# Kernel optimization log

Measured on AMD Instinct MI355X. Metric: run time of the kernel, lower is better.

The kernel has to match this reference:

```python
import jax, jax.numpy as jnp
import numpy as np

B, C, H, W = 256, 512, 14, 14  # C = rnn_size
S = 7                          # spp_size

def setup_inputs() -> dict:
    key = jax.random.key(0)
    ks = jax.random.split(key, 8)
    sd = 1.0 / np.sqrt(C)
    return {
        "att_v": jax.random.normal(ks[0], (B, C, H, W), dtype=jnp.float32),
        "h": jax.random.normal(ks[1], (B, C), dtype=jnp.float32),
        # a2a: Linear(rnn_size, rnn_size)
        "Wa": jax.random.uniform(ks[2], (C, C), jnp.float32, -sd, sd),
        "ba": jax.random.uniform(ks[3], (C,), jnp.float32, -sd, sd),
        # h2a: Linear(rnn_size, rnn_size)
        "Wh": jax.random.uniform(ks[4], (C, C), jnp.float32, -sd, sd),
        "bh": jax.random.uniform(ks[5], (C,), jnp.float32, -sd, sd),
        # d2d: Linear(rnn_size, 1)
        "Wd": jax.random.uniform(ks[6], (C,), jnp.float32, -sd, sd),
        "bd": jax.random.uniform(ks[7], (1,), jnp.float32, -sd, sd),
    }

def reference(att_v, h, Wa, ba, Wh, bh, Wd, bd):
    b, c, hh, ww = att_v.shape
    # AdaptiveAvgPool2d(S) with H,W divisible by S -> block mean
    pooled = att_v.reshape(b, c, S, hh // S, S, ww // S).mean(axis=(3, 5))  # [B,C,S,S]
    a = pooled.reshape(b, c, S * S).transpose(0, 2, 1)  # [B, N=49, C]
    av = jnp.einsum('bnc,dc->bnd', a, Wa) + ba          # a2a, torch Linear: x @ W.T + b
    ah = h @ Wh.T + bh                                  # h2a, [B,C]
    dot = jnp.tanh(av + ah[:, None, :])                 # broadcast add + tanh
    scores = jnp.einsum('bnd,d->bn', dot, Wd) + bd[0]   # d2d -> [B, N]
    weight = jax.nn.softmax(scores, axis=-1)            # over attention positions
    att_res = jnp.einsum('bnc,bn->bc', a, weight)       # bmm(att^T, weight)
    return att_res
```

## Files before the change

kernel.cpp:

```cpp
#include <hip/hip_runtime.h>
#include <hip/hip_bf16.h>

#define BATCH 256
#define CDIM  512
#define NPOS  49
#define MROWS 12544
#define ASTRIDE 520

typedef __attribute__((ext_vector_type(8))) short bf16x8_t;
typedef __attribute__((ext_vector_type(4))) float f32x4_t;

#define WS_NEED 14730240u

__device__ __forceinline__ void load_lds16(const void* g, void* l) {
    __builtin_amdgcn_global_load_lds(
        (const __attribute__((address_space(1))) void*)g,
        (__attribute__((address_space(3))) void*)l, 16, 0, 0);
}

__global__ __launch_bounds__(256) void prep(
    const float* __restrict__ Wa, const float* __restrict__ Wh,
    const float* __restrict__ h,
    __hip_bfloat16* __restrict__ Wab, __hip_bfloat16* __restrict__ Whb,
    __hip_bfloat16* __restrict__ hb, float* __restrict__ scores) {
    int gid = blockIdx.x * 256 + threadIdx.x;
    if (gid >= 166976) return;
    if (gid < 163840) {
        const float* src; __hip_bfloat16* dst; int idx;
        if (gid < 65536)       { src = Wa; dst = Wab; idx = gid; }
        else if (gid < 131072) { src = Wh; dst = Whb; idx = gid - 65536; }
        else                   { src = h;  dst = hb;  idx = gid - 131072; }
        float4 v = ((const float4*)src)[idx];
        dst[idx * 4 + 0] = __float2bfloat16(v.x);
        dst[idx * 4 + 1] = __float2bfloat16(v.y);
        dst[idx * 4 + 2] = __float2bfloat16(v.z);
        dst[idx * 4 + 3] = __float2bfloat16(v.w);
    } else {
        int idx = gid - 163840;
        ((float4*)scores)[idx] = (float4){0.f, 0.f, 0.f, 0.f};
    }
}

__global__ __launch_bounds__(256, 6) void pool_kernel(
    const float* __restrict__ att_v, __hip_bfloat16* __restrict__ pooled) {
    __shared__ float4 lds[32 * 49];
    const int b  = blockIdx.x >> 4;
    const int cg = blockIdx.x & 15;
    const int t  = threadIdx.x;

    const float4* src = (const float4*)(att_v + ((size_t)b * CDIM + cg * 32) * 196);
    #pragma unroll
    for (int k = 0; k < 7; ++k) {
        int idx = t + k * 256;
        if (idx < 1568) lds[idx] = src[idx];
    }
    __syncthreads();

    const int i = t >> 5;
    const int c = t & 31;
    if (i < 7) {
        const float4* fp = &lds[c * 49 + 7 * i];
        float4 f0 = fp[0], f1 = fp[1], f2 = fp[2], f3 = fp[3];
        float4 f4 = fp[4], f5 = fp[5], f6 = fp[6];
        float p[7];
        p[0] = f0.x + f0.y + f3.z + f3.w;
        p[1] = f0.z + f0.w + f4.x + f4.y;
        p[2] = f1.x + f1.y + f4.z + f4.w;
        p[3] = f1.z + f1.w + f5.x + f5.y;
        p[4] = f2.x + f2.y + f5.z + f5.w;
        p[5] = f2.z + f2.w + f6.x + f6.y;
        p[6] = f3.x + f3.y + f6.z + f6.w;
        __hip_bfloat16* outp = pooled + ((size_t)b * NPOS + i * 7) * CDIM + cg * 32 + c;
        #pragma unroll
        for (int j = 0; j < 7; ++j)
            outp[(size_t)j * CDIM] = __float2bfloat16(p[j] * 0.25f);
    }
}

__global__ __launch_bounds__(256, 2) void ah_gemm(
    const __hip_bfloat16* __restrict__ A,
    const __hip_bfloat16* __restrict__ Bw,
    const float* __restrict__ ba, const float* __restrict__ bh,
    float* __restrict__ ahb) {
    __shared__ __hip_bfloat16 aT[128 * 32];
    __shared__ __hip_bfloat16 bT[128 * 32];
    const int mt = blockIdx.x & 1;
    const int nt = blockIdx.x >> 1;
    const int t = threadIdx.x;
    const int wave = t >> 6, lane = t & 63;
    const int wm = wave & 1, wn = wave >> 1;
    const int q = lane >> 4, r = lane & 15;
    const int m0 = mt * 128, n0 = nt * 128;

    const __hip_bfloat16* Ag = A + (size_t)(m0 + wave * 16 + (lane >> 2)) * CDIM + (lane & 3) * 8;
    const __hip_bfloat16* Bg = Bw + (size_t)(n0 + wave * 16 + (lane >> 2)) * CDIM + (lane & 3) * 8;
    char* aD = (char*)aT + wave * 1024 + lane * 16;
    char* bD = (char*)bT + wave * 1024 + lane * 16;

    f32x4_t acc[4][4];
    #pragma unroll
    for (int rt = 0; rt < 4; ++rt)
        #pragma unroll
        for (int ct = 0; ct < 4; ++ct) acc[rt][ct] = (f32x4_t){0.f, 0.f, 0.f, 0.f};

    for (int ks = 0; ks < 16; ++ks) {
        const __hip_bfloat16* ag = Ag + ks * 32;
        const __hip_bfloat16* bg = Bg + ks * 32;
        load_lds16(ag, aD);
        load_lds16(ag + 64 * CDIM, aD + 4096);
        load_lds16(bg, bD);
        load_lds16(bg + 64 * CDIM, bD + 4096);
        __syncthreads();
        bf16x8_t af[4], bf[4];
        #pragma unroll
        for (int rt = 0; rt < 4; ++rt)
            af[rt] = *(const bf16x8_t*)&aT[(wm * 64 + rt * 16 + r) * 32 + q * 8];
        #pragma unroll
        for (int ct = 0; ct < 4; ++ct)
            bf[ct] = *(const bf16x8_t*)&bT[(wn * 64 + ct * 16 + r) * 32 + q * 8];
        #pragma unroll
        for (int rt = 0; rt < 4; ++rt)
            #pragma unroll
            for (int ct = 0; ct < 4; ++ct)
                acc[rt][ct] = __builtin_amdgcn_mfma_f32_16x16x32_bf16(
                    af[rt], bf[ct], acc[rt][ct], 0, 0, 0);
        __syncthreads();
    }
    #pragma unroll
    for (int ct = 0; ct < 4; ++ct) {
        const int col = n0 + wn * 64 + ct * 16 + r;
        const float bias = ba[col] + bh[col];
        #pragma unroll
        for (int rt = 0; rt < 4; ++rt)
            #pragma unroll
            for (int rg = 0; rg < 4; ++rg) {
                const int row = m0 + wm * 64 + rt * 16 + q * 4 + rg;
                ahb[(size_t)row * CDIM + col] = acc[rt][ct][rg] + bias;
            }
    }
}

__global__ __launch_bounds__(256, 2) void gemm_score2(
    const __hip_bfloat16* __restrict__ A,
    const __hip_bfloat16* __restrict__ Bw,
    const float* __restrict__ ahb,
    const float* __restrict__ Wd,
    float* __restrict__ scores) {
    __shared__ __hip_bfloat16 aT[128 * 32];
    __shared__ __hip_bfloat16 bT[128 * 32];
    const int mt = blockIdx.x % 98;
    const int nt = blockIdx.x / 98;
    const int t = threadIdx.x;
    const int wave = t >> 6, lane = t & 63;
    const int wm = wave & 1, wn = wave >> 1;
    const int q = lane >> 4, r = lane & 15;
    const int m0 = mt * 128, n0 = nt * 128;

    const __hip_bfloat16* Ag = A + (size_t)(m0 + wave * 16 + (lane >> 2)) * CDIM + (lane & 3) * 8;
    const __hip_bfloat16* Bg = Bw + (size_t)(n0 + wave * 16 + (lane >> 2)) * CDIM + (lane & 3) * 8;
    char* aD = (char*)aT + wave * 1024 + lane * 16;
    char* bD = (char*)bT + wave * 1024 + lane * 16;

    f32x4_t acc[4][4];
    #pragma unroll
    for (int rt = 0; rt < 4; ++rt)
        #pragma unroll
        for (int ct = 0; ct < 4; ++ct) acc[rt][ct] = (f32x4_t){0.f, 0.f, 0.f, 0.f};

    for (int ks = 0; ks < 16; ++ks) {
        const __hip_bfloat16* ag = Ag + ks * 32;
        const __hip_bfloat16* bg = Bg + ks * 32;
        load_lds16(ag, aD);
        load_lds16(ag + 64 * CDIM, aD + 4096);
        load_lds16(bg, bD);
        load_lds16(bg + 64 * CDIM, bD + 4096);
        __syncthreads();
        bf16x8_t af[4], bf[4];
        #pragma unroll
        for (int rt = 0; rt < 4; ++rt)
            af[rt] = *(const bf16x8_t*)&aT[(wm * 64 + rt * 16 + r) * 32 + q * 8];
        #pragma unroll
        for (int ct = 0; ct < 4; ++ct)
            bf[ct] = *(const bf16x8_t*)&bT[(wn * 64 + ct * 16 + r) * 32 + q * 8];
        #pragma unroll
        for (int rt = 0; rt < 4; ++rt)
            #pragma unroll
            for (int ct = 0; ct < 4; ++ct)
                acc[rt][ct] = __builtin_amdgcn_mfma_f32_16x16x32_bf16(
                    af[rt], bf[ct], acc[rt][ct], 0, 0, 0);
        __syncthreads();
    }

    int bb[16];
    #pragma unroll
    for (int rt = 0; rt < 4; ++rt)
        #pragma unroll
        for (int rg = 0; rg < 4; ++rg)
            bb[rt * 4 + rg] = (m0 + wm * 64 + rt * 16 + q * 4 + rg) / NPOS;

    float rsum[16];
    #pragma unroll
    for (int i = 0; i < 16; ++i) rsum[i] = 0.f;

    #pragma unroll
    for (int ct = 0; ct < 4; ++ct) {
        const int col = n0 + wn * 64 + ct * 16 + r;
        const float wd = Wd[col];
        #pragma unroll
        for (int rt = 0; rt < 4; ++rt)
            #pragma unroll
            for (int rg = 0; rg < 4; ++rg) {
                float x = acc[rt][ct][rg] + ahb[(size_t)bb[rt * 4 + rg] * CDIM + col];
                float e = __expf(2.f * x);
                rsum[rt * 4 + rg] += (1.f - 2.f / (e + 1.f)) * wd;
            }
    }
    #pragma unroll
    for (int m = 1; m < 16; m <<= 1)
        #pragma unroll
        for (int i = 0; i < 16; ++i)
            rsum[i] += __shfl_xor(rsum[i], m, 64);
    if (r == 0) {
        #pragma unroll
        for (int rt = 0; rt < 4; ++rt)
            #pragma unroll
            for (int rg = 0; rg < 4; ++rg)
                atomicAdd(&scores[m0 + wm * 64 + rt * 16 + q * 4 + rg],
                          rsum[rt * 4 + rg]);
    }
}

__global__ __launch_bounds__(256) void softmax_wsum(
    const float* __restrict__ scores, const __hip_bfloat16* __restrict__ pooled,
    float* __restrict__ out) {
    const int b  = blockIdx.x >> 1;
    const int ch = (blockIdx.x & 1) * 256 + threadIdx.x;
    const float* sp = scores + b * NPOS;
    float vmax = -3.0e38f;
    #pragma unroll
    for (int n = 0; n < NPOS; ++n) vmax = fmaxf(vmax, sp[n]);
    const __hip_bfloat16* Ap = pooled + (size_t)b * NPOS * CDIM + ch;
    float sum = 0.f, accv = 0.f;
    #pragma unroll
    for (int n = 0; n < NPOS; ++n) {
        float e = __expf(sp[n] - vmax);
        sum += e;
        accv += e * __bfloat162float(Ap[(size_t)n * CDIM]);
    }
    out[b * CDIM + ch] = accv / sum;
}

__global__ void prep_convert(const float* __restrict__ Wa,
                             const float* __restrict__ Wh,
                             __hip_bfloat16* __restrict__ Wab,
                             __hip_bfloat16* __restrict__ Whb) {
    int gid = blockIdx.x * blockDim.x + threadIdx.x;
    const int quarter = (CDIM * CDIM) / 4;
    const float4* src; __hip_bfloat16* dst; int idx;
    if (gid < quarter) { src = (const float4*)Wa; dst = Wab; idx = gid; }
    else               { src = (const float4*)Wh; dst = Whb; idx = gid - quarter; }
    float4 v = src[idx];
    dst[idx * 4 + 0] = __float2bfloat16(v.x);
    dst[idx * 4 + 1] = __float2bfloat16(v.y);
    dst[idx * 4 + 2] = __float2bfloat16(v.z);
    dst[idx * 4 + 3] = __float2bfloat16(v.w);
}

__global__ __launch_bounds__(512, 2) void att_spp_main(
    const float* __restrict__ att_v, const float* __restrict__ h,
    const float* __restrict__ ba, const float* __restrict__ bh,
    const float* __restrict__ Wd,
    const __hip_bfloat16* __restrict__ Wab, const __hip_bfloat16* __restrict__ Whb,
    float* __restrict__ out) {
    __shared__ __hip_bfloat16 a_lds[64 * ASTRIDE];
    __shared__ __hip_bfloat16 h_lds[CDIM];
    __shared__ float babh_lds[CDIM];
    __shared__ float wd_lds[CDIM];
    __shared__ float scores_lds[64];
    __shared__ float weights_lds[NPOS];
    const int b = blockIdx.x, t = threadIdx.x;
    h_lds[t]    = __float2bfloat16(h[b * CDIM + t]);
    babh_lds[t] = ba[t] + bh[t];
    wd_lds[t]   = Wd[t];
    if (t < 64) scores_lds[t] = 0.f;
    for (int idx = t; idx < (64 - NPOS) * ASTRIDE; idx += 512)
        a_lds[NPOS * ASTRIDE + idx] = __float2bfloat16(0.f);
    {
        const int jj = t & 7, g = t >> 3;
        const float2* att2 = (const float2*)(att_v + (size_t)b * CDIM * 196);
        if (jj < 7) {
            for (int ci = 0; ci < 8; ++ci) {
                const int c = g + (ci << 6), cbase = c * 98;
                #pragma unroll
                for (int i = 0; i < 7; ++i) {
                    float2 v0 = att2[cbase + i * 14 + jj];
                    float2 v1 = att2[cbase + i * 14 + 7 + jj];
                    a_lds[(i * 7 + jj) * ASTRIDE + c] =
                        __float2bfloat16((v0.x + v0.y + v1.x + v1.y) * 0.25f);
                }
            }
        }
    }
    __syncthreads();
    const int wave = t >> 6, lane = t & 63, q = lane >> 4, r = lane & 15;
    f32x4_t acc[4][4];
    #pragma unroll
    for (int rt = 0; rt < 4; ++rt)
        #pragma unroll
        for (int ct = 0; ct < 4; ++ct) acc[rt][ct] = (f32x4_t){0.f,0.f,0.f,0.f};
    const int dBase = wave * 64 + r;
    for (int ks = 0; ks < 16; ++ks) {
        const int k0 = ks * 32 + q * 8;
        bf16x8_t af[4], bf[4];
        #pragma unroll
        for (int rt = 0; rt < 4; ++rt)
            af[rt] = *(const bf16x8_t*)&a_lds[(rt * 16 + r) * ASTRIDE + k0];
        #pragma unroll
        for (int ct = 0; ct < 4; ++ct)
            bf[ct] = *(const bf16x8_t*)&Wab[(size_t)(dBase + ct * 16) * CDIM + k0];
        #pragma unroll
        for (int rt = 0; rt < 4; ++rt)
            #pragma unroll
            for (int ct = 0; ct < 4; ++ct)
                acc[rt][ct] = __builtin_amdgcn_mfma_f32_16x16x32_bf16(
                    af[rt], bf[ct], acc[rt][ct], 0, 0, 0);
    }
    for (int ks = 0; ks < 16; ++ks) {
        const int k0 = ks * 32 + q * 8;
        bf16x8_t af = *(const bf16x8_t*)&h_lds[k0];
        bf16x8_t bf[4];
        #pragma unroll
        for (int ct = 0; ct < 4; ++ct)
            bf[ct] = *(const bf16x8_t*)&Whb[(size_t)(dBase + ct * 16) * CDIM + k0];
        #pragma unroll
        for (int rt = 0; rt < 4; ++rt)
            #pragma unroll
            for (int ct = 0; ct < 4; ++ct)
                acc[rt][ct] = __builtin_amdgcn_mfma_f32_16x16x32_bf16(
                    af, bf[ct], acc[rt][ct], 0, 0, 0);
    }
    float part[4][4];
    #pragma unroll
    for (int rt = 0; rt < 4; ++rt)
        #pragma unroll
        for (int rg = 0; rg < 4; ++rg) part[rt][rg] = 0.f;
    #pragma unroll
    for (int ct = 0; ct < 4; ++ct) {
        const int d = dBase + ct * 16;
        const float bias = babh_lds[d], wd = wd_lds[d];
        #pragma unroll
        for (int rt = 0; rt < 4; ++rt)
            #pragma unroll
            for (int rg = 0; rg < 4; ++rg) {
                float x = acc[rt][ct][rg] + bias;
                float e = __expf(2.f * x);
                part[rt][rg] += (1.f - 2.f / (e + 1.f)) * wd;
            }
    }
    #pragma unroll
    for (int m = 1; m < 16; m <<= 1)
        #pragma unroll
        for (int rt = 0; rt < 4; ++rt)
            #pragma unroll
            for (int rg = 0; rg < 4; ++rg)
                part[rt][rg] += __shfl_xor(part[rt][rg], m, 64);
    if (r == 0) {
        #pragma unroll
        for (int rt = 0; rt < 4; ++rt)
            #pragma unroll
            for (int rg = 0; rg < 4; ++rg)
                atomicAdd(&scores_lds[rt * 16 + q * 4 + rg], part[rt][rg]);
    }
    __syncthreads();
    if (wave == 0) {
        float v = (lane < NPOS) ? scores_lds[lane] : -3.0e38f;
        float vmax = v;
        #pragma unroll
        for (int m = 1; m < 64; m <<= 1) vmax = fmaxf(vmax, __shfl_xor(vmax, m, 64));
        float e = (lane < NPOS) ? __expf(v - vmax) : 0.f;
        float s = e;
        #pragma unroll
        for (int m = 1; m < 64; m <<= 1) s += __shfl_xor(s, m, 64);
        if (lane < NPOS) weights_lds[lane] = e / s;
    }
    __syncthreads();
    float sum = 0.f;
    #pragma unroll
    for (int n = 0; n < NPOS; ++n)
        sum += __bfloat162float(a_lds[n * ASTRIDE + t]) * weights_lds[n];
    out[b * CDIM + t] = sum;
}

extern "C" void kernel_launch(void* const* d_in, const int* in_sizes, int n_in,
                              void* d_out, int out_size, void* d_ws, size_t ws_size,
                              hipStream_t stream) {
    const float* att_v = (const float*)d_in[0];
    const float* h     = (const float*)d_in[1];
    const float* Wa    = (const float*)d_in[2];
    const float* ba    = (const float*)d_in[3];
    const float* Wh    = (const float*)d_in[4];
    const float* bh    = (const float*)d_in[5];
    const float* Wd    = (const float*)d_in[6];

    if (ws_size >= WS_NEED) {
        char* ws = (char*)d_ws;
        __hip_bfloat16* Wab    = (__hip_bfloat16*)(ws);
        __hip_bfloat16* Whb    = (__hip_bfloat16*)(ws + 524288);
        __hip_bfloat16* hb     = (__hip_bfloat16*)(ws + 1048576);
        __hip_bfloat16* pooled = (__hip_bfloat16*)(ws + 1310720);
        float*          ahb    = (float*)(ws + 14155776);
        float*          scores = (float*)(ws + 14680064);

        prep<<<653, 256, 0, stream>>>(Wa, Wh, h, Wab, Whb, hb, scores);
        pool_kernel<<<4096, 256, 0, stream>>>(att_v, pooled);
        ah_gemm<<<8, 256, 0, stream>>>(hb, Whb, ba, bh, ahb);
        gemm_score2<<<392, 256, 0, stream>>>(pooled, Wab, ahb, Wd, scores);
        softmax_wsum<<<512, 256, 0, stream>>>(scores, pooled, (float*)d_out);
    } else {
        __hip_bfloat16* Wab = (__hip_bfloat16*)d_ws;
        __hip_bfloat16* Whb = Wab + (size_t)CDIM * CDIM;
        prep_convert<<<512, 256, 0, stream>>>(Wa, Wh, Wab, Whb);
        att_spp_main<<<BATCH, 512, 0, stream>>>(att_v, h, ba, bh, Wd, Wab, Whb,
                                                (float*)d_out);
    }
}
```

Baseline: 200.6 us.

## Tile score GEMM per batch and replace atomics with partial-score buffers

The score GEMM now uses one 64-row tile per batch (49 valid rows) across 4 N-tiles, so each block reads a single ah row instead of gathering per-row batch indices. Atomics into a zeroed scores array are replaced by 8 per-wave-column partial segments that the softmax kernel sums into LDS, which removes the zeroing pass from prep. The ah GEMM switches to 64x64 tiles so it runs on 32 blocks instead of 8. The cost is padding 49 rows up to 64, about 23% wasted MFMA and load work, plus a larger workspace.

```diff
diff --git a/kernel.cpp b/kernel.cpp
--- a/kernel.cpp
+++ b/kernel.cpp
@@ -10,7 +10,7 @@
 typedef __attribute__((ext_vector_type(8))) short bf16x8_t;
 typedef __attribute__((ext_vector_type(4))) float f32x4_t;
 
-#define WS_NEED 14730240u
+#define WS_NEED 15081472u
 
 __device__ __forceinline__ void load_lds16(const void* g, void* l) {
     __builtin_amdgcn_global_load_lds(
@@ -22,23 +22,17 @@
     const float* __restrict__ Wa, const float* __restrict__ Wh,
     const float* __restrict__ h,
     __hip_bfloat16* __restrict__ Wab, __hip_bfloat16* __restrict__ Whb,
-    __hip_bfloat16* __restrict__ hb, float* __restrict__ scores) {
+    __hip_bfloat16* __restrict__ hb) {
     int gid = blockIdx.x * 256 + threadIdx.x;
-    if (gid >= 166976) return;
-    if (gid < 163840) {
-        const float* src; __hip_bfloat16* dst; int idx;
-        if (gid < 65536)       { src = Wa; dst = Wab; idx = gid; }
-        else if (gid < 131072) { src = Wh; dst = Whb; idx = gid - 65536; }
-        else                   { src = h;  dst = hb;  idx = gid - 131072; }
-        float4 v = ((const float4*)src)[idx];
-        dst[idx * 4 + 0] = __float2bfloat16(v.x);
-        dst[idx * 4 + 1] = __float2bfloat16(v.y);
-        dst[idx * 4 + 2] = __float2bfloat16(v.z);
-        dst[idx * 4 + 3] = __float2bfloat16(v.w);
-    } else {
-        int idx = gid - 163840;
-        ((float4*)scores)[idx] = (float4){0.f, 0.f, 0.f, 0.f};
-    }
+    const float* src; __hip_bfloat16* dst; int idx;
+    if (gid < 65536)       { src = Wa; dst = Wab; idx = gid; }
+    else if (gid < 131072) { src = Wh; dst = Whb; idx = gid - 65536; }
+    else                   { src = h;  dst = hb;  idx = gid - 131072; }
+    float4 v = ((const float4*)src)[idx];
+    dst[idx * 4 + 0] = __float2bfloat16(v.x);
+    dst[idx * 4 + 1] = __float2bfloat16(v.y);
+    dst[idx * 4 + 2] = __float2bfloat16(v.z);
+    dst[idx * 4 + 3] = __float2bfloat16(v.w);
 }
 
 __global__ __launch_bounds__(256, 6) void pool_kernel(
@@ -77,173 +71,176 @@
     }
 }
 
-__global__ __launch_bounds__(256, 2) void ah_gemm(
+__global__ __launch_bounds__(256, 4) void ah_gemm(
     const __hip_bfloat16* __restrict__ A,
     const __hip_bfloat16* __restrict__ Bw,
     const float* __restrict__ ba, const float* __restrict__ bh,
     float* __restrict__ ahb) {
-    __shared__ __hip_bfloat16 aT[128 * 32];
-    __shared__ __hip_bfloat16 bT[128 * 32];
-    const int mt = blockIdx.x & 1;
-    const int nt = blockIdx.x >> 1;
+    __shared__ __hip_bfloat16 aT[64 * 32];
+    __shared__ __hip_bfloat16 bT[64 * 32];
+    const int mt = blockIdx.x & 3;
+    const int nt = blockIdx.x >> 2;
     const int t = threadIdx.x;
     const int wave = t >> 6, lane = t & 63;
     const int wm = wave & 1, wn = wave >> 1;
     const int q = lane >> 4, r = lane & 15;
-    const int m0 = mt * 128, n0 = nt * 128;
-
-    const __hip_bfloat16* Ag = A + (size_t)(m0 + wave * 16 + (lane >> 2)) * CDIM + (lane & 3) * 8;
-    const __hip_bfloat16* Bg = Bw + (size_t)(n0 + wave * 16 + (lane >> 2)) * CDIM + (lane & 3) * 8;
-    char* aD = (char*)aT + wave * 1024 + lane * 16;
-    char* bD = (char*)bT + wave * 1024 + lane * 16;
-
-    f32x4_t acc[4][4];
-    #pragma unroll
-    for (int rt = 0; rt < 4; ++rt)
+    const int m0 = mt * 64, n0 = nt * 64;
+
+    const __hip_bfloat16* Ag = A + (size_t)(m0 + (t >> 2)) * CDIM + (t & 3) * 8;
+    const __hip_bfloat16* Bg = Bw + (size_t)(n0 + (t >> 2)) * CDIM + (t & 3) * 8;
+    char* aD = (char*)aT + t * 16;
+    char* bD = (char*)bT + t * 16;
+
+    f32x4_t acc[2][2];
+    #pragma unroll
+    for (int rt = 0; rt < 2; ++rt)
+        #pragma unroll
+        for (int ct = 0; ct < 2; ++ct) acc[rt][ct] = (f32x4_t){0.f, 0.f, 0.f, 0.f};
+
+    for (int ks = 0; ks < 16; ++ks) {
+        load_lds16(Ag + ks * 32, aD);
+        load_lds16(Bg + ks * 32, bD);
+        __syncthreads();
+        bf16x8_t af[2], bf[2];
+        #pragma unroll
+        for (int rt = 0; rt < 2; ++rt)
+            af[rt] = *(const bf16x8_t*)&aT[(wm * 32 + rt * 16 + r) * 32 + q * 8];
+        #pragma unroll
+        for (int ct = 0; ct < 2; ++ct)
+            bf[ct] = *(const bf16x8_t*)&bT[(wn * 32 + ct * 16 + r) * 32 + q * 8];
+        #pragma unroll
+        for (int rt = 0; rt < 2; ++rt)
+            #pragma unroll
+            for (int ct = 0; ct < 2; ++ct)
+                acc[rt][ct] = __builtin_amdgcn_mfma_f32_16x16x32_bf16(
+                    af[rt], bf[ct], acc[rt][ct], 0, 0, 0);
+        __syncthreads();
+    }
+    #pragma unroll
+    for (int ct = 0; ct < 2; ++ct) {
+        const int col = n0 + wn * 32 + ct * 16 + r;
+        const float bias = ba[col] + bh[col];
+        #pragma unroll
+        for (int rt = 0; rt < 2; ++rt)
+            #pragma unroll
+            for (int rg = 0; rg < 4; ++rg) {
+                const int row = m0 + wm * 32 + rt * 16 + q * 4 + rg;
+                ahb[(size_t)row * CDIM + col] = acc[rt][ct][rg] + bias;
+            }
+    }
+}
+
+__global__ __launch_bounds__(256, 4) void gemm_score3(
+    const __hip_bfloat16* __restrict__ A,
+    const __hip_bfloat16* __restrict__ Bw,
+    const float* __restrict__ ahb,
+    const float* __restrict__ Wd,
+    float* __restrict__ scores8) {
+    __shared__ __hip_bfloat16 aT[64 * 32];
+    __shared__ __hip_bfloat16 bT[128 * 32];
+    const int b  = blockIdx.x >> 2;
+    const int nt = blockIdx.x & 3;
+    const int t = threadIdx.x;
+    const int wave = t >> 6, lane = t & 63;
+    const int wm = wave & 1, wn = wave >> 1;
+    const int q = lane >> 4, r = lane & 15;
+    const int m0 = b * NPOS;
+    const int n0 = nt * 128;
+
+    const __hip_bfloat16* Ag = A + (size_t)(m0 + (t >> 2)) * CDIM + (t & 3) * 8;
+    const __hip_bfloat16* Bg = Bw + (size_t)(n0 + (t >> 2)) * CDIM + (t & 3) * 8;
+    char* aD = (char*)aT + t * 16;
+    char* bD = (char*)bT + t * 16;
+
+    f32x4_t acc[2][4];
+    #pragma unroll
+    for (int rt = 0; rt < 2; ++rt)
         #pragma unroll
         for (int ct = 0; ct < 4; ++ct) acc[rt][ct] = (f32x4_t){0.f, 0.f, 0.f, 0.f};
 
     for (int ks = 0; ks < 16; ++ks) {
-        const __hip_bfloat16* ag = Ag + ks * 32;
-        const __hip_bfloat16* bg = Bg + ks * 32;
-        load_lds16(ag, aD);
-        load_lds16(ag + 64 * CDIM, aD + 4096);
-        load_lds16(bg, bD);
-        load_lds16(bg + 64 * CDIM, bD + 4096);
+        load_lds16(Ag + ks * 32, aD);
+        load_lds16(Bg + ks * 32, bD);
+        load_lds16(Bg + (size_t)64 * CDIM + ks * 32, bD + 4096);
         __syncthreads();
-        bf16x8_t af[4], bf[4];
-        #pragma unroll
-        for (int rt = 0; rt < 4; ++rt)
-            af[rt] = *(const bf16x8_t*)&aT[(wm * 64 + rt * 16 + r) * 32 + q * 8];
+        bf16x8_t af[2], bf[4];
+        #pragma unroll
+        for (int rt = 0; rt < 2; ++rt)
+            af[rt] = *(const bf16x8_t*)&aT[(wm * 32 + rt * 16 + r) * 32 + q * 8];
         #pragma unroll
         for (int ct = 0; ct < 4; ++ct)
             bf[ct] = *(const bf16x8_t*)&bT[(wn * 64 + ct * 16 + r) * 32 + q * 8];
         #pragma unroll
-        for (int rt = 0; rt < 4; ++rt)
+        for (int rt = 0; rt < 2; ++rt)
             #pragma unroll
             for (int ct = 0; ct < 4; ++ct)
                 acc[rt][ct] = __builtin_amdgcn_mfma_f32_16x16x32_bf16(
                     af[rt], bf[ct], acc[rt][ct], 0, 0, 0);
         __syncthreads();
     }
+
+    float rsum[2][4];
+    #pragma unroll
+    for (int rt = 0; rt < 2; ++rt)
+        #pragma unroll
+        for (int rg = 0; rg < 4; ++rg) rsum[rt][rg] = 0.f;
+
+    const float* ahp = ahb + (size_t)b * CDIM;
     #pragma unroll
     for (int ct = 0; ct < 4; ++ct) {
         const int col = n0 + wn * 64 + ct * 16 + r;
-        const float bias = ba[col] + bh[col];
-        #pragma unroll
-        for (int rt = 0; rt < 4; ++rt)
+        const float ah = ahp[col];
+        const float wd = Wd[col];
+        #pragma unroll
+        for (int rt = 0; rt < 2; ++rt)
             #pragma unroll
             for (int rg = 0; rg < 4; ++rg) {
-                const int row = m0 + wm * 64 + rt * 16 + q * 4 + rg;
-                ahb[(size_t)row * CDIM + col] = acc[rt][ct][rg] + bias;
+                float x = acc[rt][ct][rg] + ah;
+                float e = __expf(2.f * x);
+                rsum[rt][rg] += (1.f - 2.f / (e + 1.f)) * wd;
             }
     }
-}
-
-__global__ __launch_bounds__(256, 2) void gemm_score2(
-    const __hip_bfloat16* __restrict__ A,
-    const __hip_bfloat16* __restrict__ Bw,
-    const float* __restrict__ ahb,
-    const float* __restrict__ Wd,
-    float* __restrict__ scores) {
-    __shared__ __hip_bfloat16 aT[128 * 32];
-    __shared__ __hip_bfloat16 bT[128 * 32];
-    const int mt = blockIdx.x % 98;
-    const int nt = blockIdx.x / 98;
-    const int t = threadIdx.x;
-    const int wave = t >> 6, lane = t & 63;
-    const int wm = wave & 1, wn = wave >> 1;
-    const int q = lane >> 4, r = lane & 15;
-    const int m0 = mt * 128, n0 = nt * 128;
-
-    const __hip_bfloat16* Ag = A + (size_t)(m0 + wave * 16 + (lane >> 2)) * CDIM + (lane & 3) * 8;
-    const __hip_bfloat16* Bg = Bw + (size_t)(n0 + wave * 16 + (lane >> 2)) * CDIM + (lane & 3) * 8;
-    char* aD = (char*)aT + wave * 1024 + lane * 16;
-    char* bD = (char*)bT + wave * 1024 + lane * 16;
-
-    f32x4_t acc[4][4];
-    #pragma unroll
-    for (int rt = 0; rt < 4; ++rt)
-        #pragma unroll
-        for (int ct = 0; ct < 4; ++ct) acc[rt][ct] = (f32x4_t){0.f, 0.f, 0.f, 0.f};
-
-    for (int ks = 0; ks < 16; ++ks) {
-        const __hip_bfloat16* ag = Ag + ks * 32;
-        const __hip_bfloat16* bg = Bg + ks * 32;
-        load_lds16(ag, aD);
-        load_lds16(ag + 64 * CDIM, aD + 4096);
-        load_lds16(bg, bD);
-        load_lds16(bg + 64 * CDIM, bD + 4096);
-        __syncthreads();
-        bf16x8_t af[4], bf[4];
-        #pragma unroll
-        for (int rt = 0; rt < 4; ++rt)
-            af[rt] = *(const bf16x8_t*)&aT[(wm * 64 + rt * 16 + r) * 32 + q * 8];
-        #pragma unroll
-        for (int ct = 0; ct < 4; ++ct)
-            bf[ct] = *(const bf16x8_t*)&bT[(wn * 64 + ct * 16 + r) * 32 + q * 8];
-        #pragma unroll
-        for (int rt = 0; rt < 4; ++rt)
-            #pragma unroll
-            for (int ct = 0; ct < 4; ++ct)
-                acc[rt][ct] = __builtin_amdgcn_mfma_f32_16x16x32_bf16(
-                    af[rt], bf[ct], acc[rt][ct], 0, 0, 0);
-        __syncthreads();
-    }
-
-    int bb[16];
-    #pragma unroll
-    for (int rt = 0; rt < 4; ++rt)
-        #pragma unroll
-        for (int rg = 0; rg < 4; ++rg)
-            bb[rt * 4 + rg] = (m0 + wm * 64 + rt * 16 + q * 4 + rg) / NPOS;
-
-    float rsum[16];
-    #pragma unroll
-    for (int i = 0; i < 16; ++i) rsum[i] = 0.f;
-
-    #pragma unroll
-    for (int ct = 0; ct < 4; ++ct) {
-        const int col = n0 + wn * 64 + ct * 16 + r;
-        const float wd = Wd[col];
-        #pragma unroll
-        for (int rt = 0; rt < 4; ++rt)
+    #pragma unroll
+    for (int m = 1; m < 16; m <<= 1)
+        #pragma unroll
+        for (int rt = 0; rt < 2; ++rt)
+            #pragma unroll
+            for (int rg = 0; rg < 4; ++rg)
+                rsum[rt][rg] += __shfl_xor(rsum[rt][rg], m, 64);
+    if (r == 0) {
+        float* seg = scores8 + (size_t)(nt * 2 + wn) * MROWS + m0;
+        #pragma unroll
+        for (int rt = 0; rt < 2; ++rt)
             #pragma unroll
             for (int rg = 0; rg < 4; ++rg) {
-                float x = acc[rt][ct][rg] + ahb[(size_t)bb[rt * 4 + rg] * CDIM + col];
-                float e = __expf(2.f * x);
-                rsum[rt * 4 + rg] += (1.f - 2.f / (e + 1.f)) * wd;
+                const int row = wm * 32 + rt * 16 + q * 4 + rg;
+                if (row < NPOS) seg[row] = rsum[rt][rg];
             }
     }
-    #pragma unroll
-    for (int m = 1; m < 16; m <<= 1)
-        #pragma unroll
-        for (int i = 0; i < 16; ++i)
-            rsum[i] += __shfl_xor(rsum[i], m, 64);
-    if (r == 0) {
-        #pragma unroll
-        for (int rt = 0; rt < 4; ++rt)
-            #pragma unroll
-            for (int rg = 0; rg < 4; ++rg)
-                atomicAdd(&scores[m0 + wm * 64 + rt * 16 + q * 4 + rg],
-                          rsum[rt * 4 + rg]);
-    }
 }
 
 __global__ __launch_bounds__(256) void softmax_wsum(
-    const float* __restrict__ scores, const __hip_bfloat16* __restrict__ pooled,
+    const float* __restrict__ scores8, const __hip_bfloat16* __restrict__ pooled,
     float* __restrict__ out) {
+    __shared__ float s_lds[NPOS];
     const int b  = blockIdx.x >> 1;
     const int ch = (blockIdx.x & 1) * 256 + threadIdx.x;
-    const float* sp = scores + b * NPOS;
+    if (threadIdx.x < NPOS) {
+        float s = 0.f;
+        #pragma unroll
+        for (int seg = 0; seg < 8; ++seg)
+            s += scores8[(size_t)seg * MROWS + b * NPOS + threadIdx.x];
+        s_lds[threadIdx.x] = s;
+    }
+    __syncthreads();
     float vmax = -3.0e38f;
     #pragma unroll
-    for (int n = 0; n < NPOS; ++n) vmax = fmaxf(vmax, sp[n]);
+    for (int n = 0; n < NPOS; ++n) vmax = fmaxf(vmax, s_lds[n]);
     const __hip_bfloat16* Ap = pooled + (size_t)b * NPOS * CDIM + ch;
     float sum = 0.f, accv = 0.f;
     #pragma unroll
     for (int n = 0; n < NPOS; ++n) {
-        float e = __expf(sp[n] - vmax);
+        float e = __expf(s_lds[n] - vmax);
         sum += e;
         accv += e * __bfloat162float(Ap[(size_t)n * CDIM]);
     }
@@ -404,18 +401,18 @@
 
     if (ws_size >= WS_NEED) {
         char* ws = (char*)d_ws;
-        __hip_bfloat16* Wab    = (__hip_bfloat16*)(ws);
-        __hip_bfloat16* Whb    = (__hip_bfloat16*)(ws + 524288);
-        __hip_bfloat16* hb     = (__hip_bfloat16*)(ws + 1048576);
-        __hip_bfloat16* pooled = (__hip_bfloat16*)(ws + 1310720);
-        float*          ahb    = (float*)(ws + 14155776);
-        float*          scores = (float*)(ws + 14680064);
-
-        prep<<<653, 256, 0, stream>>>(Wa, Wh, h, Wab, Whb, hb, scores);
+        __hip_bfloat16* Wab     = (__hip_bfloat16*)(ws);
+        __hip_bfloat16* Whb     = (__hip_bfloat16*)(ws + 524288);
+        __hip_bfloat16* hb      = (__hip_bfloat16*)(ws + 1048576);
+        __hip_bfloat16* pooled  = (__hip_bfloat16*)(ws + 1310720);
+        float*          ahb     = (float*)(ws + 14155776);
+        float*          scores8 = (float*)(ws + 14680064);
+
+        prep<<<640, 256, 0, stream>>>(Wa, Wh, h, Wab, Whb, hb);
         pool_kernel<<<4096, 256, 0, stream>>>(att_v, pooled);
-        ah_gemm<<<8, 256, 0, stream>>>(hb, Whb, ba, bh, ahb);
-        gemm_score2<<<392, 256, 0, stream>>>(pooled, Wab, ahb, Wd, scores);
-        softmax_wsum<<<512, 256, 0, stream>>>(scores, pooled, (float*)d_out);
+        ah_gemm<<<32, 256, 0, stream>>>(hb, Whb, ba, bh, ahb);
+        gemm_score3<<<1024, 256, 0, stream>>>(pooled, Wab, ahb, Wd, scores8);
+        softmax_wsum<<<512, 256, 0, stream>>>(scores8, pooled, (float*)d_out);
     } else {
         __hip_bfloat16* Wab = (__hip_bfloat16*)d_ws;
         __hip_bfloat16* Whb = Wab + (size_t)CDIM * CDIM;
```

After: 198.8 us. Within noise of the previous version (-0.9%).
